# Optimization experiments

Measured on AMD Instinct MI355X. Metric: run time of the kernel, lower is better.

Reference implementation:

```python
import jax, jax.numpy as jnp
import numpy as np

B, C, NUM_CLASSES = 1, 64, 20
D, H, W = 128, 128, 32
THRES = 0.2
EPS = 1e-5


def _instance_norm(x, gamma, beta):
    # InstanceNorm3d: normalize each (batch, channel) over spatial dims, affine.
    mean = jnp.mean(x, axis=(2, 3, 4), keepdims=True)
    var = jnp.var(x, axis=(2, 3, 4), keepdims=True)
    xhat = (x - mean) * jax.lax.rsqrt(var + EPS)
    return gamma[None, :, None, None, None] * xhat + beta[None, :, None, None, None]


def setup_inputs() -> dict:
    key = jax.random.key(0)
    k0, k1, k2 = jax.random.split(key, 3)
    x = jax.random.normal(k0, (B, C, D, H, W), jnp.float32)
    # classifier: Conv3d(C, NUM_CLASSES, kernel_size=1) with bias
    cls_w = jax.random.normal(k1, (NUM_CLASSES, C), jnp.float32) * 0.05
    cls_b = jnp.zeros((NUM_CLASSES,), jnp.float32)
    # CFR branches: NUM_CLASSES x Conv3d(3, 1, k=7, pad=3, no bias) -> stacked [K,1,3,7,7,7]
    cfr_w = jax.random.normal(k2, (NUM_CLASSES, 1, 3, 7, 7, 7), jnp.float32) * 0.05
    # InstanceNorm3d affine params
    in_gamma = jnp.ones((C,), jnp.float32)
    in_beta = jnp.zeros((C,), jnp.float32)
    return {"x": x, "cls_w": cls_w, "cls_b": cls_b, "cfr_w": cfr_w,
            "in_gamma": in_gamma, "in_beta": in_beta}


def _forward(x, cls_w, cls_b, cfr_w, in_gamma, in_beta):
    # classifier on detached x (1x1x1 conv == channel matmul)
    xd = jax.lax.stop_gradient(x)
    logit = jnp.einsum('bcdhw,oc->bodhw', xd, cls_w) + cls_b[None, :, None, None, None]
    masks = jax.nn.softmax(logit, axis=1)  # [B,K,D,H,W]

    acc = jnp.zeros_like(x)
    for i in range(NUM_CLASSES):
        mask = masks[:, i:i + 1]                 # [B,1,D,H,W]
        mid = x * mask                           # [B,C,D,H,W]
        avg_out = jnp.mean(mid, axis=1, keepdims=True)
        max_out = jnp.max(mid, axis=1, keepdims=True)
        atten_in = jnp.concatenate([avg_out, max_out, mask], axis=1)  # [B,3,D,H,W]
        conv = jax.lax.conv_general_dilated(
            atten_in, cfr_w[i], window_strides=(1, 1, 1),
            padding=[(3, 3), (3, 3), (3, 3)],
            dimension_numbers=('NCDHW', 'OIDHW', 'NCDHW'))  # [B,1,D,H,W]
        atten = jax.nn.sigmoid(conv)
        out = mid * atten
        # class-region mask from globally min-max-normalized heatmap
        heat = jnp.mean(out, axis=1, keepdims=True)
        norm = (heat - heat.min()) / (heat.max() - heat.min())
        region = (norm > THRES).astype(x.dtype)
        out = _instance_norm(out * region, in_gamma, in_beta)
        acc = acc + out
    out_ = jax.nn.relu(acc)
    return out_, logit


def reference(x, cls_w, cls_b, cfr_w, in_gamma, in_beta):
    return _forward(x, cls_w, cls_b, cfr_w, in_gamma, in_beta)
```

## Files before the change

kernel.cpp:

```cpp
#include <hip/hip_runtime.h>

#define VOX (128*128*32)
#define CCH 64
#define NCL 20
#define DD 128
#define HH 128
#define WW 32
#define ZT 8
#define EPSV 1e-5f
#define THRESV 0.2f

__device__ __forceinline__ unsigned keyOf(float f){
    unsigned u = __float_as_uint(f);
    return (u & 0x80000000u) ? ~u : (u | 0x80000000u);
}
__device__ __forceinline__ float keyInv(unsigned k){
    unsigned u = (k & 0x80000000u) ? (k & 0x7fffffffu) : ~k;
    return __uint_as_float(u);
}

__global__ void k_init(unsigned* keys, float* zpg){
    int i = threadIdx.x;
    if (i < NCL){ keys[i] = 0xFFFFFFFFu; keys[NCL+i] = 0u; }
    #pragma unroll
    for (int k = 0; k < 4; ++k) zpg[k*64 + i] = 0.f;
}

__global__ __launch_bounds__(256) void k_logit_softmax(
    const float* __restrict__ x, const float* __restrict__ clsw,
    const float* __restrict__ clsb, float* __restrict__ masks,
    float* __restrict__ logit, float* __restrict__ mx, float* __restrict__ Mx)
{
    __shared__ float sw[NCL*CCH];
    __shared__ float sb[NCL];
    int tid = threadIdx.x;
    for (int q = tid; q < NCL*CCH; q += 256) sw[q] = clsw[q];
    if (tid < NCL) sb[tid] = clsb[tid];
    __syncthreads();
    int v = blockIdx.x*256 + tid;
    float acc[NCL];
    #pragma unroll
    for (int o=0;o<NCL;o++) acc[o] = sb[o];
    float s = 0.f, mm = -1e30f;
    for (int c=0;c<CCH;c++){
        float xv = x[c*VOX + v];
        s += xv; mm = fmaxf(mm, xv);
        #pragma unroll
        for (int o=0;o<NCL;o++) acc[o] = fmaf(xv, sw[o*CCH + c], acc[o]);
    }
    mx[v] = s * (1.f/64.f);
    Mx[v] = mm;
    float lm = acc[0];
    #pragma unroll
    for (int o=1;o<NCL;o++) lm = fmaxf(lm, acc[o]);
    float es = 0.f;
    #pragma unroll
    for (int o=0;o<NCL;o++){
        logit[o*VOX + v] = acc[o];
        float e = expf(acc[o] - lm);
        es += e; acc[o] = e;
    }
    float inv = 1.f/es;
    #pragma unroll
    for (int o=0;o<NCL;o++) masks[o*VOX + v] = acc[o]*inv;
}


#define F4(A, WV, q0,q1,q2,q3) { A.x=fmaf(q0,WV,A.x); A.y=fmaf(q1,WV,A.y); \
                                 A.z=fmaf(q2,WV,A.z); A.w=fmaf(q3,WV,A.w); }
#define DZ4(A, WP, P) { \
    F4(A,(WP)[0], P##0,P##1,P##2,P##3) \
    F4(A,(WP)[1], P##1,P##2,P##3,P##4) \
    F4(A,(WP)[2], P##2,P##3,P##4,P##5) \
    F4(A,(WP)[3], P##3,P##4,P##5,P##6) \
    F4(A,(WP)[4], P##4,P##5,P##6,P##7) \
    F4(A,(WP)[5], P##5,P##6,P##7,P##8) \
    F4(A,(WP)[6], P##6,P##7,P##8,P##9) }

#define TGROUP4(P, WT) { \
    const float* wd_ = (WT) + dy*7; \
    if (ok6) DZ4(a6, wd_+0,   P) \
    if (ok5) DZ4(a5, wd_+49,  P) \
    if (ok4) DZ4(a4, wd_+98,  P) \
    if (ok3) DZ4(a3, wd_+147, P) \
    if (ok2) DZ4(a2, wd_+196, P) \
    if (ok1) DZ4(a1, wd_+245, P) \
    if (ok0) DZ4(a0, wd_+294, P) }

#define PLANE_F 1280
#define BUF_F   3840
#define LDS_F   7680

__device__ __forceinline__ void issue_slice(const float* mk, const float* mxp, const float* Mxp,
        const float* zpg, float* FLf, int bufF, int zi, int y0, int lane, int wid)
{
    const bool zok = (unsigned)zi < (unsigned)DD;
    const float* srcs[3] = { mk, mxp, Mxp };
    #pragma unroll
    for (int k = 0; k < 15; ++k){
        if ((k >> 2) != wid) continue;
        const int f = k/5, j = k%5;
        int Q   = j*64 + lane;
        int row = Q >> 3, xq = Q & 7;
        int gy  = y0 - 3 + row;
        const float* g;
        if (zok && row < 38 && (unsigned)gy < (unsigned)HH)
            g = srcs[f] + ((size_t)(zi*HH + gy)*32 + xq*4);
        else
            g = zpg + lane*4;
        float* l = FLf + bufF + f*PLANE_F + j*256;
        __builtin_amdgcn_global_load_lds(
            (const __attribute__((address_space(1))) void*)g,
            (__attribute__((address_space(3))) void*)l, 16, 0, 0);
    }
}

__global__ __launch_bounds__(256, 5) void k_conv12(const float* __restrict__ masksAll,
        const float* __restrict__ mxp, const float* __restrict__ Mxp,
        const float* __restrict__ cfr, float* __restrict__ G,
        unsigned* __restrict__ keys, const float* __restrict__ zpg)
{
    __shared__ __align__(16) float FLf[LDS_F];
    __shared__ float r4[8];
    const int y0  = blockIdx.x * 32;
    const int z0  = blockIdx.y * ZT;
    const int cls = blockIdx.z;
    const int tid = threadIdx.x;
    const int lane = tid & 63, wid = tid >> 6;
    const int y  = tid >> 3;
    const int xg = tid & 7;
    const int x0 = xg * 4;
    const bool lo_inv = (xg == 0), hi_inv = (xg == 7);
    const float* mk   = masksAll + (size_t)cls * VOX;
    const float* wcls = cfr + cls*1029;
    float* Gc = G + (size_t)cls * VOX;

    issue_slice(mk, mxp, Mxp, zpg, FLf, 0,     z0-3, y0, lane, wid);
    issue_slice(mk, mxp, Mxp, zpg, FLf, BUF_F, z0-2, y0, lane, wid);

    float4 a0{},a1{},a2{},a3{},a4{},a5{},a6{};
    float4 g0m{},g0x{},g1m{},g1x{},g2m{},g2x{};
    float hmn = 1e30f, hmx = -1e30f;
    int cur = 0;

    #pragma unroll 1
    for (int zi = z0 - 3; zi <= z0 + ZT + 2; ++zi){
        const bool pst = (zi >= z0 + 4);
        if (wid == 3){ if (pst) asm volatile("s_waitcnt vmcnt(4)" ::: "memory");
                       else     asm volatile("s_waitcnt vmcnt(3)" ::: "memory"); }
        else         { if (pst) asm volatile("s_waitcnt vmcnt(5)" ::: "memory");
                       else     asm volatile("s_waitcnt vmcnt(4)" ::: "memory"); }
        __builtin_amdgcn_sched_barrier(0);
        __builtin_amdgcn_s_barrier();
        __builtin_amdgcn_sched_barrier(0);

        const bool cap = (zi >= z0 && zi < z0 + ZT);
        float4 nm{}, nx{};

        const int lo = z0 + 3 - zi;
        const bool ok0 = (0>=lo) && (0-lo<ZT);
        const bool ok1 = (1>=lo) && (1-lo<ZT);
        const bool ok2 = (2>=lo) && (2-lo<ZT);
        const bool ok3 = (3>=lo) && (3-lo<ZT);
        const bool ok4 = (4>=lo) && (4-lo<ZT);
        const bool ok5 = (5>=lo) && (5-lo<ZT);
        const bool ok6 = (6>=lo) && (6-lo<ZT);

        #pragma unroll 1
        for (int dy = 0; dy < 7; ++dy){
            const int r = y + dy;
            const float* Pm = FLf + cur*BUF_F + r*32;
            const float* Pa = Pm + PLANE_F;
            const float* Pb = Pa + PLANE_F;
            const int c0 = (xg > 0 ? xg-1 : 0)*4;
            const int c1 = xg*4;
            const int c2 = (xg < 7 ? xg+1 : 7)*4;
            const float4 M0 = *(const float4*)(Pm + c0);
            const float4 M1 = *(const float4*)(Pm + c1);
            const float4 M2 = *(const float4*)(Pm + c2);
            if (cap && dy == 3) nm = M1;
            const float pm0 = lo_inv ? 0.f : M0.y;
            const float pm1 = lo_inv ? 0.f : M0.z;
            const float pm2 = lo_inv ? 0.f : M0.w;
            const float pm3 = M1.x, pm4 = M1.y, pm5 = M1.z, pm6 = M1.w;
            const float pm7 = hi_inv ? 0.f : M2.x;
            const float pm8 = hi_inv ? 0.f : M2.y;
            const float pm9 = hi_inv ? 0.f : M2.z;

            {
                const float4 A0 = *(const float4*)(Pa + c0);
                const float4 A1 = *(const float4*)(Pa + c1);
                const float4 A2 = *(const float4*)(Pa + c2);
                if (cap && dy == 3) nx = A1;
                const float pa0 = pm0*A0.y, pa1 = pm1*A0.z, pa2 = pm2*A0.w;
                const float pa3 = pm3*A1.x, pa4 = pm4*A1.y, pa5 = pm5*A1.z, pa6 = pm6*A1.w;
                const float pa7 = pm7*A2.x, pa8 = pm8*A2.y, pa9 = pm9*A2.z;
                TGROUP4(pa, wcls)
            }
            {
                const float4 B0 = *(const float4*)(Pb + c0);
                const float4 B1 = *(const float4*)(Pb + c1);
                const float4 B2 = *(const float4*)(Pb + c2);
                const float pb0 = pm0*B0.y, pb1 = pm1*B0.z, pb2 = pm2*B0.w;
                const float pb3 = pm3*B1.x, pb4 = pm4*B1.y, pb5 = pm5*B1.z, pb6 = pm6*B1.w;
                const float pb7 = pm7*B2.x, pb8 = pm8*B2.y, pb9 = pm9*B2.z;
                TGROUP4(pb, wcls + 343)
            }
            TGROUP4(pm, wcls + 686)
        }

        __builtin_amdgcn_sched_barrier(0);
        __builtin_amdgcn_s_barrier();
        __builtin_amdgcn_sched_barrier(0);
        issue_slice(mk, mxp, Mxp, zpg, FLf, cur*BUF_F, zi+2, y0, lane, wid);
        __builtin_amdgcn_sched_barrier(0);

        if (zi >= z0 + 3){
            const int zo = zi - 3;
            const int oidx = (zo*HH + (y0 + y))*WW + x0;
            float4 r1;
            r1.x = g0m.x/(1.f + expf(-a0.x));
            r1.y = g0m.y/(1.f + expf(-a0.y));
            r1.z = g0m.z/(1.f + expf(-a0.z));
            r1.w = g0m.w/(1.f + expf(-a0.w));
            *(float4*)(Gc + oidx) = r1;
            float h0 = r1.x*g0x.x, h1 = r1.y*g0x.y, h2 = r1.z*g0x.z, h3 = r1.w*g0x.w;
            hmn = fminf(hmn, fminf(fminf(h0,h1), fminf(h2,h3)));
            hmx = fmaxf(hmx, fmaxf(fmaxf(h0,h1), fmaxf(h2,h3)));
        }
        a0=a1; a1=a2; a2=a3; a3=a4; a4=a5; a5=a6;
        a6 = make_float4(0.f,0.f,0.f,0.f);
        g0m=g1m; g0x=g1x; g1m=g2m; g1x=g2x; g2m=nm; g2x=nx;
        cur ^= 1;
    }
    asm volatile("s_waitcnt vmcnt(0)" ::: "memory");

    #pragma unroll
    for (int off = 32; off > 0; off >>= 1){
        hmn = fminf(hmn, __shfl_xor(hmn, off));
        hmx = fmaxf(hmx, __shfl_xor(hmx, off));
    }
    if ((tid & 63) == 0){ r4[wid*2] = hmn; r4[wid*2+1] = hmx; }
    __syncthreads();
    if (tid == 0){
        float a = fminf(fminf(r4[0],r4[2]), fminf(r4[4],r4[6]));
        float b = fmaxf(fmaxf(r4[1],r4[3]), fmaxf(r4[5],r4[7]));
        atomicMin(&keys[cls],     keyOf(a));
        atomicMax(&keys[NCL+cls], keyOf(b));
    }
}

__global__ void k_thr(const unsigned* __restrict__ keys, float* __restrict__ hminA,
                      float* __restrict__ invR){
    int i = threadIdx.x;
    if (i < NCL){
        float hm = keyInv(keys[i]);
        float hM = keyInv(keys[NCL+i]);
        hminA[i] = hm;
        invR[i] = 1.f/(hM - hm);
    }
}

__global__ __launch_bounds__(256) void k_region(float* G, const float* __restrict__ mx,
        const float* __restrict__ hminA, const float* __restrict__ invR)
{
    int i = blockIdx.y;
    int v = blockIdx.x*256 + threadIdx.x;
    float ma = G[i*VOX + v];
    float heat = ma * mx[v];
    float norm = (heat - hminA[i]) * invR[i];
    G[i*VOX + v] = (norm > THRESV) ? ma : 0.f;
}

__global__ __launch_bounds__(256) void k_stats(const float* __restrict__ x,
        const float* G, float* __restrict__ part)
{
    __shared__ float xt[64][65];
    int tid = threadIdx.x;
    int c = tid & 63, vg = tid >> 6;
    int v0 = blockIdx.x * 2048;
    const int cc = tid >> 2;
    const int u0 = (tid & 3) * 16;
    float s1[NCL], s2[NCL];
    #pragma unroll
    for (int i=0;i<NCL;i++){ s1[i]=0.f; s2[i]=0.f; }
    #pragma unroll 1
    for (int t = 0; t < 32; ++t){
        int vb = v0 + t*64;
        __syncthreads();
        float ld[16];
        #pragma unroll
        for (int j = 0; j < 4; ++j){
            float4 f4 = *(const float4*)&x[(size_t)cc*VOX + vb + u0 + j*4];
            ld[j*4+0]=f4.x; ld[j*4+1]=f4.y; ld[j*4+2]=f4.z; ld[j*4+3]=f4.w;
        }
        #pragma unroll
        for (int j = 0; j < 16; ++j) xt[u0 + j][cc] = ld[j];
        __syncthreads();
        #pragma unroll 1
        for (int k = 0; k < 16; ++k){
            int vv = (k<<2) + vg;
            float xv = xt[vv][c];
            #pragma unroll
            for (int i=0;i<NCL;i++){
                float p = xv * G[i*VOX + vb + vv];
                s1[i] += p;
                s2[i] = fmaf(p, p, s2[i]);
            }
        }
    }
    __shared__ float red[4][64][2*NCL];
    #pragma unroll
    for (int i=0;i<NCL;i++){ red[vg][c][i] = s1[i]; red[vg][c][NCL+i] = s2[i]; }
    __syncthreads();
    if (vg == 0){
        float* dst = part + (size_t)blockIdx.x * (NCL*CCH*2);
        for (int i=0;i<NCL;i++){
            float a = red[0][c][i]+red[1][c][i]+red[2][c][i]+red[3][c][i];
            float b = red[0][c][NCL+i]+red[1][c][NCL+i]+red[2][c][NCL+i]+red[3][c][NCL+i];
            dst[i*CCH*2 + c*2 + 0] = a;
            dst[i*CCH*2 + c*2 + 1] = b;
        }
    }
}

__global__ void k_params(const float* __restrict__ part, const float* __restrict__ gamma,
        const float* __restrict__ beta, float* __restrict__ aArr, float* __restrict__ kcArr)
{
    int i = blockIdx.x, c = threadIdx.x;
    float s1 = 0.f, s2 = 0.f;
    for (int b=0;b<256;b++){
        const float* p = part + (size_t)b*(NCL*CCH*2) + i*CCH*2 + c*2;
        s1 += p[0]; s2 += p[1];
    }
    float m   = s1 * (1.f/(float)VOX);
    float var = s2 * (1.f/(float)VOX) - m*m;
    float rinv = 1.f/sqrtf(var + EPSV);
    float gm = gamma[c];
    aArr[i*CCH + c]  = gm*rinv;
    kcArr[i*CCH + c] = beta[c] - m*rinv*gm;
}

__global__ void k_kcol(const float* __restrict__ kcArr, float* __restrict__ KcA){
    int c = threadIdx.x;
    if (c < CCH){
        float s = 0.f;
        for (int i=0;i<NCL;i++) s += kcArr[i*CCH + c];
        KcA[c] = s;
    }
}

__global__ __launch_bounds__(256) void k_final(const float* __restrict__ x,
        float* outAll, const float* __restrict__ aArr, const float* __restrict__ KcA)
{
    __shared__ float aL[NCL*CCH];
    __shared__ float KL[CCH];
    int tid = threadIdx.x;
    for (int q=tid; q<NCL*CCH; q+=256) aL[q] = aArr[q];
    if (tid < CCH) KL[tid] = KcA[tid];
    __syncthreads();
    int v = blockIdx.x*256 + tid;
    const float* Gp = outAll + (size_t)NCL*VOX;
    float g[NCL];
    #pragma unroll
    for (int i=0;i<NCL;i++) g[i] = Gp[i*VOX + v];
    #pragma unroll 4
    for (int c=0;c<CCH;c++){
        float P = 0.f;
        #pragma unroll
        for (int i=0;i<NCL;i++) P = fmaf(g[i], aL[i*CCH + c], P);
        float xv = x[c*VOX + v];
        outAll[c*VOX + v] = fmaxf(0.f, fmaf(xv, P, KL[c]));
    }
}

extern "C" void kernel_launch(void* const* d_in, const int* in_sizes, int n_in,
                              void* d_out, int out_size, void* d_ws, size_t ws_size,
                              hipStream_t stream)
{
    const float* x     = (const float*)d_in[0];
    const float* clsw  = (const float*)d_in[1];
    const float* clsb  = (const float*)d_in[2];
    const float* cfr   = (const float*)d_in[3];
    const float* gamma = (const float*)d_in[4];
    const float* beta  = (const float*)d_in[5];

    float* out   = (float*)d_out;
    float* logit = out + (size_t)CCH*VOX;
    float* masks = out;
    float* G     = out + (size_t)NCL*VOX;

    float* ws    = (float*)d_ws;
    float* mxp   = ws;
    float* Mxp   = ws + VOX;
    unsigned* keys = (unsigned*)(ws + 2*(size_t)VOX);
    float* hminA = ws + 2*(size_t)VOX + 64;
    float* invR  = hminA + NCL;
    float* part  = ws + 2*(size_t)VOX + 128;
    float* aArr  = part + 256*(NCL*CCH*2);
    float* kcArr = aArr + NCL*CCH;
    float* KcA   = kcArr + NCL*CCH;
    float* zpg   = KcA + CCH;

    k_init<<<1, 64, 0, stream>>>(keys, zpg);
    k_logit_softmax<<<VOX/256, 256, 0, stream>>>(x, clsw, clsb, masks, logit, mxp, Mxp);
    k_conv12<<<dim3(4, 16, NCL), 256, 0, stream>>>(masks, mxp, Mxp, cfr, G, keys, zpg);
    k_thr<<<1, 32, 0, stream>>>(keys, hminA, invR);
    k_region<<<dim3(VOX/256, NCL), 256, 0, stream>>>(G, mxp, hminA, invR);
    k_stats<<<256, 256, 0, stream>>>(x, G, part);
    k_params<<<NCL, CCH, 0, stream>>>(part, gamma, beta, aArr, kcArr);
    k_kcol<<<1, CCH, 0, stream>>>(kcArr, KcA);
    k_final<<<VOX/256, 256, 0, stream>>>(x, out, aArr, KcA);
}
```

Before: 745.4 us.

## Vectorize logit softmax, double per-thread work in final, split stats finer, raise conv priority

```diff
diff --git a/kernel.cpp b/kernel.cpp
--- a/kernel.cpp
+++ b/kernel.cpp
@@ -26,7 +26,7 @@
     for (int k = 0; k < 4; ++k) zpg[k*64 + i] = 0.f;
 }
 
-__global__ __launch_bounds__(256) void k_logit_softmax(
+__global__ __launch_bounds__(256, 4) void k_logit_softmax(
     const float* __restrict__ x, const float* __restrict__ clsw,
     const float* __restrict__ clsb, float* __restrict__ masks,
     float* __restrict__ logit, float* __restrict__ mx, float* __restrict__ Mx)
@@ -37,34 +37,53 @@
     for (int q = tid; q < NCL*CCH; q += 256) sw[q] = clsw[q];
     if (tid < NCL) sb[tid] = clsb[tid];
     __syncthreads();
-    int v = blockIdx.x*256 + tid;
-    float acc[NCL];
-    #pragma unroll
-    for (int o=0;o<NCL;o++) acc[o] = sb[o];
-    float s = 0.f, mm = -1e30f;
+    const int v = blockIdx.x*1024 + tid*4;
+    float4 acc[NCL];
+    #pragma unroll
+    for (int o=0;o<NCL;o++){ float b = sb[o]; acc[o] = make_float4(b,b,b,b); }
+    float4 s  = make_float4(0.f,0.f,0.f,0.f);
+    float4 mm = make_float4(-1e30f,-1e30f,-1e30f,-1e30f);
     for (int c=0;c<CCH;c++){
-        float xv = x[c*VOX + v];
-        s += xv; mm = fmaxf(mm, xv);
+        float4 xv = *(const float4*)&x[(size_t)c*VOX + v];
+        s.x += xv.x; s.y += xv.y; s.z += xv.z; s.w += xv.w;
+        mm.x = fmaxf(mm.x, xv.x); mm.y = fmaxf(mm.y, xv.y);
+        mm.z = fmaxf(mm.z, xv.z); mm.w = fmaxf(mm.w, xv.w);
         #pragma unroll
-        for (int o=0;o<NCL;o++) acc[o] = fmaf(xv, sw[o*CCH + c], acc[o]);
-    }
-    mx[v] = s * (1.f/64.f);
-    Mx[v] = mm;
-    float lm = acc[0];
-    #pragma unroll
-    for (int o=1;o<NCL;o++) lm = fmaxf(lm, acc[o]);
-    float es = 0.f;
+        for (int o=0;o<NCL;o++){
+            float w = sw[o*CCH + c];
+            acc[o].x = fmaf(xv.x, w, acc[o].x);
+            acc[o].y = fmaf(xv.y, w, acc[o].y);
+            acc[o].z = fmaf(xv.z, w, acc[o].z);
+            acc[o].w = fmaf(xv.w, w, acc[o].w);
+        }
+    }
+    *(float4*)&mx[v] = make_float4(s.x*(1.f/64.f), s.y*(1.f/64.f), s.z*(1.f/64.f), s.w*(1.f/64.f));
+    *(float4*)&Mx[v] = mm;
+    float4 lm = acc[0];
+    #pragma unroll
+    for (int o=1;o<NCL;o++){
+        lm.x = fmaxf(lm.x, acc[o].x); lm.y = fmaxf(lm.y, acc[o].y);
+        lm.z = fmaxf(lm.z, acc[o].z); lm.w = fmaxf(lm.w, acc[o].w);
+    }
+    float4 es = make_float4(0.f,0.f,0.f,0.f);
     #pragma unroll
     for (int o=0;o<NCL;o++){
-        logit[o*VOX + v] = acc[o];
-        float e = expf(acc[o] - lm);
-        es += e; acc[o] = e;
-    }
-    float inv = 1.f/es;
-    #pragma unroll
-    for (int o=0;o<NCL;o++) masks[o*VOX + v] = acc[o]*inv;
-}
-
+        *(float4*)&logit[(size_t)o*VOX + v] = acc[o];
+        float4 e;
+        e.x = expf(acc[o].x - lm.x); e.y = expf(acc[o].y - lm.y);
+        e.z = expf(acc[o].z - lm.z); e.w = expf(acc[o].w - lm.w);
+        es.x += e.x; es.y += e.y; es.z += e.z; es.w += e.w;
+        acc[o] = e;
+    }
+    float4 inv = make_float4(1.f/es.x, 1.f/es.y, 1.f/es.z, 1.f/es.w);
+    #pragma unroll
+    for (int o=0;o<NCL;o++){
+        float4 r;
+        r.x = acc[o].x*inv.x; r.y = acc[o].y*inv.y;
+        r.z = acc[o].z*inv.z; r.w = acc[o].w*inv.w;
+        *(float4*)&masks[(size_t)o*VOX + v] = r;
+    }
+}
 
 #define F4(A, WV, q0,q1,q2,q3) { A.x=fmaf(q0,WV,A.x); A.y=fmaf(q1,WV,A.y); \
                                  A.z=fmaf(q2,WV,A.z); A.w=fmaf(q3,WV,A.w); }
@@ -115,7 +134,7 @@
     }
 }
 
-__global__ __launch_bounds__(256, 5) void k_conv12(const float* __restrict__ masksAll,
+__global__ __launch_bounds__(256, 5) void k_conv13(const float* __restrict__ masksAll,
         const float* __restrict__ mxp, const float* __restrict__ Mxp,
         const float* __restrict__ cfr, float* __restrict__ G,
         unsigned* __restrict__ keys, const float* __restrict__ zpg)
@@ -166,6 +185,7 @@
         const bool ok5 = (5>=lo) && (5-lo<ZT);
         const bool ok6 = (6>=lo) && (6-lo<ZT);
 
+        __builtin_amdgcn_s_setprio(1);
         #pragma unroll 1
         for (int dy = 0; dy < 7; ++dy){
             const int r = y + dy;
@@ -208,6 +228,7 @@
             }
             TGROUP4(pm, wcls + 686)
         }
+        __builtin_amdgcn_s_setprio(0);
 
         __builtin_amdgcn_sched_barrier(0);
         __builtin_amdgcn_s_barrier();
@@ -278,14 +299,14 @@
     __shared__ float xt[64][65];
     int tid = threadIdx.x;
     int c = tid & 63, vg = tid >> 6;
-    int v0 = blockIdx.x * 2048;
+    int v0 = blockIdx.x * 1024;
     const int cc = tid >> 2;
     const int u0 = (tid & 3) * 16;
     float s1[NCL], s2[NCL];
     #pragma unroll
     for (int i=0;i<NCL;i++){ s1[i]=0.f; s2[i]=0.f; }
     #pragma unroll 1
-    for (int t = 0; t < 32; ++t){
+    for (int t = 0; t < 16; ++t){
         int vb = v0 + t*64;
         __syncthreads();
         float ld[16];
@@ -329,7 +350,7 @@
 {
     int i = blockIdx.x, c = threadIdx.x;
     float s1 = 0.f, s2 = 0.f;
-    for (int b=0;b<256;b++){
+    for (int b=0;b<512;b++){
         const float* p = part + (size_t)b*(NCL*CCH*2) + i*CCH*2 + c*2;
         s1 += p[0]; s2 += p[1];
     }
@@ -359,18 +380,25 @@
     for (int q=tid; q<NCL*CCH; q+=256) aL[q] = aArr[q];
     if (tid < CCH) KL[tid] = KcA[tid];
     __syncthreads();
-    int v = blockIdx.x*256 + tid;
+    int v = blockIdx.x*512 + tid;
     const float* Gp = outAll + (size_t)NCL*VOX;
-    float g[NCL];
-    #pragma unroll
-    for (int i=0;i<NCL;i++) g[i] = Gp[i*VOX + v];
+    float g[NCL], h[NCL];
+    #pragma unroll
+    for (int i=0;i<NCL;i++){ g[i] = Gp[i*VOX + v]; h[i] = Gp[i*VOX + v + 256]; }
     #pragma unroll 4
     for (int c=0;c<CCH;c++){
-        float P = 0.f;
+        float P0 = 0.f, P1 = 0.f;
         #pragma unroll
-        for (int i=0;i<NCL;i++) P = fmaf(g[i], aL[i*CCH + c], P);
-        float xv = x[c*VOX + v];
-        outAll[c*VOX + v] = fmaxf(0.f, fmaf(xv, P, KL[c]));
+        for (int i=0;i<NCL;i++){
+            float a = aL[i*CCH + c];
+            P0 = fmaf(g[i], a, P0);
+            P1 = fmaf(h[i], a, P1);
+        }
+        float kl = KL[c];
+        float xv0 = x[c*VOX + v];
+        float xv1 = x[c*VOX + v + 256];
+        outAll[c*VOX + v]       = fmaxf(0.f, fmaf(xv0, P0, kl));
+        outAll[c*VOX + v + 256] = fmaxf(0.f, fmaf(xv1, P1, kl));
     }
 }
 
@@ -397,18 +425,18 @@
     float* hminA = ws + 2*(size_t)VOX + 64;
     float* invR  = hminA + NCL;
     float* part  = ws + 2*(size_t)VOX + 128;
-    float* aArr  = part + 256*(NCL*CCH*2);
+    float* aArr  = part + 512*(NCL*CCH*2);
     float* kcArr = aArr + NCL*CCH;
     float* KcA   = kcArr + NCL*CCH;
     float* zpg   = KcA + CCH;
 
     k_init<<<1, 64, 0, stream>>>(keys, zpg);
-    k_logit_softmax<<<VOX/256, 256, 0, stream>>>(x, clsw, clsb, masks, logit, mxp, Mxp);
-    k_conv12<<<dim3(4, 16, NCL), 256, 0, stream>>>(masks, mxp, Mxp, cfr, G, keys, zpg);
+    k_logit_softmax<<<VOX/1024, 256, 0, stream>>>(x, clsw, clsb, masks, logit, mxp, Mxp);
+    k_conv13<<<dim3(4, 16, NCL), 256, 0, stream>>>(masks, mxp, Mxp, cfr, G, keys, zpg);
     k_thr<<<1, 32, 0, stream>>>(keys, hminA, invR);
     k_region<<<dim3(VOX/256, NCL), 256, 0, stream>>>(G, mxp, hminA, invR);
-    k_stats<<<256, 256, 0, stream>>>(x, G, part);
+    k_stats<<<512, 256, 0, stream>>>(x, G, part);
     k_params<<<NCL, CCH, 0, stream>>>(part, gamma, beta, aArr, kcArr);
     k_kcol<<<1, CCH, 0, stream>>>(kcArr, KcA);
-    k_final<<<VOX/256, 256, 0, stream>>>(x, out, aArr, KcA);
-}
+    k_final<<<VOX/512, 256, 0, stream>>>(x, out, aArr, KcA);
+}
```

Result: faster. 643.7 us (-13.6%).
